# Performance work log

Hardware: AMD Instinct MI355X
Metric: run time of the kernel (lower is better)

The kernel has to match this reference:

```python
import jax, jax.numpy as jnp
import numpy as np

B = 4
N = 300000
GRIDS = [(64, 48, 8), (32, 24, 4), (16, 12, 2), (8, 6, 1)]
W_IMG = 640
EFF_R = 2.0 * (int(0.01 * W_IMG + 2) / W_IMG)  # 0.025, as in source
MAXV = [EFF_R, 2.0 * EFF_R, 2.0 / 24.0, 2.0 / 12.0, 2.0 / 6.0]
CIN = [3, 18, 66, 130, 130]
COUT = [16, 64, 128, 128, 128]
E_CNT = [3600000, 786432, 196608, 24576, 3072]
V_CNT = [N, 98304, 12288, 1536, 192]


def cartesian(pos, src, dst, max_value):
    # PyG Cartesian(norm=True, cat=False, max_value=mv) followed by clamp(0,1)
    cart = pos[dst] - pos[src]
    return jnp.clip(cart / (2.0 * max_value) + 0.5, 0.0, 1.0)


def spline_conv(x, src, dst, pseudo, Wk, Wr, b, num_nodes):
    # SplineConv, kernel_size=2, degree=1 B-spline over 3-D pseudo coords:
    # 8 corner weights, per-edge trilinear basis, mean aggregation + root + bias.
    p, q = pseudo, 1.0 - pseudo
    xs = x[src]  # [E, Cin] gather
    msg = jnp.zeros((src.shape[0], Wk.shape[-1]), x.dtype)
    for s in range(8):
        basis = ((p[:, 0] if s & 1 else q[:, 0])
                 * (p[:, 1] if s & 2 else q[:, 1])
                 * (p[:, 2] if s & 4 else q[:, 2]))
        msg = msg + basis[:, None] * (xs @ Wk[s])
    agg = jax.ops.segment_sum(msg, dst, num_segments=num_nodes)
    deg = jax.ops.segment_sum(jnp.ones((dst.shape[0],), x.dtype), dst, num_segments=num_nodes)
    out = agg / jnp.maximum(deg, 1.0)[:, None] + x @ Wr + b
    return jax.nn.relu(out)


def voxel_pool(x, pos, batch, grid, aggr):
    nx, ny, nt = grid
    ix = jnp.clip(jnp.floor(pos[:, 0] * nx).astype(jnp.int32), 0, nx - 1)
    iy = jnp.clip(jnp.floor(pos[:, 1] * ny).astype(jnp.int32), 0, ny - 1)
    it = jnp.clip(jnp.floor(pos[:, 2] * nt).astype(jnp.int32), 0, nt - 1)
    cluster = ((batch * nx + ix) * ny + iy) * nt + it
    V = B * nx * ny * nt
    ones = jnp.ones((x.shape[0],), x.dtype)
    cnt = jax.ops.segment_sum(ones, cluster, num_segments=V)
    posp = jax.ops.segment_sum(pos, cluster, num_segments=V) / jnp.maximum(cnt, 1.0)[:, None]
    if aggr == 'max':
        xp = jax.ops.segment_max(x, cluster, num_segments=V)
        xp = jnp.where(cnt[:, None] > 0, xp, 0.0)
    else:
        xp = jax.ops.segment_sum(x, cluster, num_segments=V) / jnp.maximum(cnt, 1.0)[:, None]
    batchp = jnp.arange(V, dtype=jnp.int32) // (nx * ny * nt)
    return xp, posp, batchp


def _forward(x, pos, batch, edges, params):
    e0 = edges[0]
    ea = cartesian(pos, e0[0], e0[1], MAXV[0])
    h = jnp.concatenate([x, pos[:, :2]], axis=1)
    Wk, Wr, bb = params[0]
    h = spline_conv(h, e0[0], e0[1], ea, Wk, Wr, bb, x.shape[0])
    h, pos, batch = voxel_pool(h, pos, batch, GRIDS[0], 'max')
    out3 = None
    for i in range(4):
        e = edges[i + 1]
        ea = cartesian(pos, e[0], e[1], MAXV[i + 1])
        h = jnp.concatenate([h, pos[:, :2]], axis=1)
        Wk, Wr, bb = params[i + 1]
        h = spline_conv(h, e[0], e[1], ea, Wk, Wr, bb, pos.shape[0])
        if i == 2:
            out3 = h  # features after layer4 (out3 scale)
        if i < 3:
            h, pos, batch = voxel_pool(h, pos, batch, GRIDS[i + 1], 'max' if i < 2 else 'mean')
    return out3, h


def setup_inputs() -> dict:
    key = jax.random.key(0)
    ks = jax.random.split(key, 40)
    inp = {}
    inp['x'] = jax.random.uniform(ks[0], (N, 1), dtype=jnp.float32)
    inp['pos'] = jax.random.uniform(ks[1], (N, 3), dtype=jnp.float32)
    inp['batch'] = jnp.sort(jax.random.randint(ks[2], (N,), 0, B, dtype=jnp.int32))
    for i in range(5):
        inp[f'e{i}'] = jax.random.randint(ks[3 + i], (2, E_CNT[i]), 0, V_CNT[i], dtype=jnp.int32)
    kidx = 8
    for i in range(5):
        scale = 1.0 / np.sqrt(8.0 * CIN[i])
        inp[f'W{i + 1}'] = scale * jax.random.normal(ks[kidx], (8, CIN[i], COUT[i]), dtype=jnp.float32); kidx += 1
        inp[f'R{i + 1}'] = scale * jax.random.normal(ks[kidx], (CIN[i], COUT[i]), dtype=jnp.float32); kidx += 1
        inp[f'b{i + 1}'] = jnp.zeros((COUT[i],), dtype=jnp.float32)
    return inp


def reference(x, pos, batch, e0, e1, e2, e3, e4,
              W1, R1, b1, W2, R2, b2, W3, R3, b3, W4, R4, b4, W5, R5, b5):
    params = [(W1, R1, b1), (W2, R2, b2), (W3, R3, b3), (W4, R4, b4), (W5, R5, b5)]
    edges = [e0, e1, e2, e3, e4]
    return _forward(x, pos, batch, edges, params)
```

## Files before the change

kernel.cpp:

```cpp
#include <hip/hip_runtime.h>
#include <cstdint>

__device__ __forceinline__ float clamp01f(float v) { return fminf(fmaxf(v, 0.0f), 1.0f); }

__device__ __forceinline__ void basis8(float p0, float p1, float p2, float* bs)
{
    float q0 = 1.f - p0, q1 = 1.f - p1, q2 = 1.f - p2;
    float t00 = q0 * q1, t10 = p0 * q1, t01 = q0 * p1, t11 = p0 * p1;
    bs[0] = t00 * q2; bs[1] = t10 * q2; bs[2] = t01 * q2; bs[3] = t11 * q2;
    bs[4] = t00 * p2; bs[5] = t10 * p2; bs[6] = t01 * p2; bs[7] = t11 * p2;
}

__global__ __launch_bounds__(256) void edge_count_kernel(
    const int* __restrict__ edst, int* __restrict__ cnt, int E)
{
    int e = blockIdx.x * 256 + threadIdx.x;
    if (e < E) atomicAdd(&cnt[__builtin_nontemporal_load(&edst[e])], 1);
}

__global__ __launch_bounds__(256) void edge_scatter_kernel(
    const int* __restrict__ esrc, const int* __restrict__ edst,
    int* __restrict__ off, int* __restrict__ srcs, int E, int rv)
{
    const int lo = (int)(blockIdx.x & 7) * rv;
    const int hi = lo + rv;
    const int base = (int)(blockIdx.x >> 3) << 10;
#pragma unroll
    for (int k = 0; k < 4; ++k) {
        int e = base + (k << 8) + threadIdx.x;
        if (e < E) {
            int d = __builtin_nontemporal_load(&edst[e]);
            if (d >= lo && d < hi) {
                int s = __builtin_nontemporal_load(&esrc[e]);
                int slot = atomicAdd(&off[d], 1);
                srcs[slot] = s;
            }
        }
    }
}

__global__ __launch_bounds__(256) void scan1_kernel(
    const int* __restrict__ cnt, int* __restrict__ off, int* __restrict__ bsum, int V)
{
    __shared__ int lds[4096];
    __shared__ int ssum[256];
    const int t = threadIdx.x;
    const int base = blockIdx.x * 4096;
    for (int i = t; i < 4096; i += 256) {
        int g = base + i;
        lds[i] = (g < V) ? cnt[g] : 0;
    }
    __syncthreads();
    int loc[16];
    int s = 0;
#pragma unroll
    for (int k = 0; k < 16; ++k) { loc[k] = s; s += lds[t * 16 + k]; }
    ssum[t] = s;
    __syncthreads();
    for (int d = 1; d < 256; d <<= 1) {
        int v = (t >= d) ? ssum[t - d] : 0;
        __syncthreads();
        ssum[t] += v;
        __syncthreads();
    }
    const int tbase = (t == 0) ? 0 : ssum[t - 1];
    if (t == 255 && bsum) bsum[blockIdx.x] = ssum[255];
#pragma unroll
    for (int k = 0; k < 16; ++k) lds[t * 16 + k] = tbase + loc[k];
    __syncthreads();
    for (int i = t; i < 4096; i += 256) {
        int g = base + i;
        if (g < V) off[g] = lds[i];
    }
}

__global__ __launch_bounds__(256) void scan_add_kernel(
    int* __restrict__ off, const int* __restrict__ bso, int V)
{
    int g = blockIdx.x * 256 + threadIdx.x;
    if (g < V) off[g] += bso[g >> 12];
}

__global__ __launch_bounds__(256) void bin_count_kernel(
    const int* __restrict__ edst, int* __restrict__ gcnt, int E, int shift)
{
    __shared__ int h[256];
    const int t = threadIdx.x;
    h[t] = 0;
    __syncthreads();
    const int base = blockIdx.x << 12;
#pragma unroll
    for (int k = 0; k < 16; ++k) {
        int e = base + (k << 8) + t;
        if (e < E) {
            int d = __builtin_nontemporal_load(&edst[e]);
            atomicAdd(&h[d >> shift], 1);
        }
    }
    __syncthreads();
    if (h[t]) atomicAdd(&gcnt[t], h[t]);
}

__global__ __launch_bounds__(256) void bin_scatter_kernel(
    const int* __restrict__ esrc, const int* __restrict__ edst,
    int* __restrict__ gcur, int* __restrict__ stD, int* __restrict__ stS,
    int E, int shift)
{
    __shared__ int d_l[4096];
    __shared__ int s_l[4096];
    __shared__ int h[256];
    __shared__ int rbase[256];
    const int t = threadIdx.x;
    h[t] = 0;
    __syncthreads();
    const int base = blockIdx.x << 12;
#pragma unroll
    for (int k = 0; k < 16; ++k) {
        int i = (k << 8) + t;
        int e = base + i;
        if (e < E) {
            int d = __builtin_nontemporal_load(&edst[e]);
            int s = __builtin_nontemporal_load(&esrc[e]);
            d_l[i] = d; s_l[i] = s;
            atomicAdd(&h[d >> shift], 1);
        }
    }
    __syncthreads();
    rbase[t] = h[t] ? atomicAdd(&gcur[t], h[t]) : 0;
    h[t] = 0;
    __syncthreads();
#pragma unroll
    for (int k = 0; k < 16; ++k) {
        int i = (k << 8) + t;
        int e = base + i;
        if (e < E) {
            int d = d_l[i];
            int b = d >> shift;
            int r = atomicAdd(&h[b], 1);
            int pos = rbase[b] + r;
            stD[pos] = d;
            stS[pos] = s_l[i];
        }
    }
}

__global__ __launch_bounds__(1024) void bucket_csr_kernel(
    const int* __restrict__ gcur, const int* __restrict__ gcnt,
    const int* __restrict__ stD, const int* __restrict__ stS,
    int* __restrict__ cnt, int* __restrict__ off, int* __restrict__ srcs,
    int V, int shift)
{
    __shared__ int h[2048];
    __shared__ int o[2048];
    __shared__ int ps[1024];
    const int t = threadIdx.x;
    const int b = blockIdx.x;
    const int v0 = b << shift;
    const int nv = min(1 << shift, V - v0);
    const int s1 = gcur[b];
    const int s0 = s1 - gcnt[b];
    h[t] = 0; h[t + 1024] = 0;
    __syncthreads();
    for (int i = s0 + t; i < s1; i += 1024)
        atomicAdd(&h[stD[i] - v0], 1);
    __syncthreads();
    int a = h[2 * t], b2 = h[2 * t + 1];
    ps[t] = a + b2;
    __syncthreads();
    for (int d = 1; d < 1024; d <<= 1) {
        int v = (t >= d) ? ps[t - d] : 0;
        __syncthreads();
        ps[t] += v;
        __syncthreads();
    }
    int pb = (t == 0) ? 0 : ps[t - 1];
    o[2 * t] = pb;
    o[2 * t + 1] = pb + a;
    __syncthreads();
    for (int i = t; i < nv; i += 1024) {
        int hv = h[i];
        cnt[v0 + i] = hv;
        off[v0 + i] = s0 + o[i] + hv;
    }
    __syncthreads();
    for (int i = s0 + t; i < s1; i += 1024) {
        int d = stD[i];
        int r = atomicAdd(&o[d - v0], 1);
        srcs[s0 + r] = stS[i];
    }
}

__global__ __launch_bounds__(256) void pack_xpos_kernel(
    const float* __restrict__ x, const float* __restrict__ pos,
    float4* __restrict__ xp, int V)
{
    int n = blockIdx.x * 256 + threadIdx.x;
    if (n >= V) return;
    xp[n] = make_float4(x[n], pos[n * 3 + 0], pos[n * 3 + 1], pos[n * 3 + 2]);
}

__device__ __forceinline__ void l1_edge_acc(
    const float4 d, const float4 a, float inv2mv, float ts[8][3])
{
    float p0 = clamp01f((d.y - a.y) * inv2mv + 0.5f);
    float p1 = clamp01f((d.z - a.z) * inv2mv + 0.5f);
    float p2 = clamp01f((d.w - a.w) * inv2mv + 0.5f);
    float bs[8];
    basis8(p0, p1, p2, bs);
#pragma unroll
    for (int s8 = 0; s8 < 8; ++s8) {
        ts[s8][0] += bs[s8] * a.x;
        ts[s8][1] += bs[s8] * a.y;
        ts[s8][2] += bs[s8] * a.z;
    }
}

__global__ __launch_bounds__(256) void l1_fused_kernel(
    const int* __restrict__ off, const int* __restrict__ cnt, const int* __restrict__ srcs,
    const float4* __restrict__ xp,
    const float* __restrict__ Wk, const float* __restrict__ Wr,
    const float* __restrict__ bias, float* __restrict__ out,
    float inv2mv, int V)
{
    __shared__ float sWk[384];
    __shared__ float sWr[48];
    __shared__ float sB[16];
    const int t = threadIdx.x;
    for (int i = t; i < 384; i += 256) sWk[i] = Wk[i];
    if (t < 48) sWr[t] = Wr[t];
    if (t < 16) sB[t] = bias[t];
    __syncthreads();
    const int v = blockIdx.x * 256 + t;
    if (v >= V) return;
    const float4 d = xp[v];
    const int e1 = off[v];
    const int n = cnt[v];
    float ts[8][3];
#pragma unroll
    for (int s8 = 0; s8 < 8; ++s8) { ts[s8][0] = 0.f; ts[s8][1] = 0.f; ts[s8][2] = 0.f; }
    int j = e1 - n;
    for (; j + 3 < e1; j += 4) {
        float4 a0 = xp[srcs[j]];
        float4 a1 = xp[srcs[j + 1]];
        float4 a2 = xp[srcs[j + 2]];
        float4 a3 = xp[srcs[j + 3]];
        l1_edge_acc(d, a0, inv2mv, ts);
        l1_edge_acc(d, a1, inv2mv, ts);
        l1_edge_acc(d, a2, inv2mv, ts);
        l1_edge_acc(d, a3, inv2mv, ts);
    }
    for (; j < e1; ++j)
        l1_edge_acc(d, xp[srcs[j]], inv2mv, ts);
    const float invn = 1.0f / fmaxf((float)n, 1.0f);
    float rr[16];
#pragma unroll
    for (int c = 0; c < 16; ++c) {
        float m = 0.f;
#pragma unroll
        for (int s8 = 0; s8 < 8; ++s8)
            m += ts[s8][0] * sWk[s8 * 48 + c]
               + ts[s8][1] * sWk[s8 * 48 + 16 + c]
               + ts[s8][2] * sWk[s8 * 48 + 32 + c];
        float r = m * invn + d.x * sWr[c] + d.y * sWr[16 + c] + d.z * sWr[32 + c] + sB[c];
        rr[c] = fmaxf(r, 0.0f);
    }
    float4* op = (float4*)(out + (size_t)v * 16);
#pragma unroll
    for (int k = 0; k < 4; ++k)
        op[k] = make_float4(rr[4 * k], rr[4 * k + 1], rr[4 * k + 2], rr[4 * k + 3]);
}

__device__ __forceinline__ void l2_edge_acc(
    const float4 pd, const float4 pa, float fa, int l16, float inv2mv,
    float* accF, float* accP)
{
    float p0 = clamp01f((pd.x - pa.x) * inv2mv + 0.5f);
    float p1 = clamp01f((pd.y - pa.y) * inv2mv + 0.5f);
    float p2 = clamp01f((pd.z - pa.z) * inv2mv + 0.5f);
    float bs[8];
    basis8(p0, p1, p2, bs);
    const float fp = (l16 == 0) ? pa.x : ((l16 == 1) ? pa.y : 0.f);
#pragma unroll
    for (int s8 = 0; s8 < 8; ++s8) {
        accF[s8] += bs[s8] * fa;
        accP[s8] += bs[s8] * fp;
    }
}

template<int NW>
__global__ __launch_bounds__(64 * NW) void tsum16_layer_kernel(
    const int* __restrict__ off, const int* __restrict__ cnt, const int* __restrict__ srcs,
    const float4* __restrict__ pos4, const float* __restrict__ feat,
    const float* __restrict__ Wk, const float* __restrict__ Wr,
    const float* __restrict__ bias, float* __restrict__ out,
    float inv2mv, int V)
{
    __shared__ float tsum[NW][4][18][9];
    const int tid = threadIdx.x;
    const int w = tid >> 6, lane = tid & 63;
    const int q = lane >> 4, l16 = lane & 15;
    const int vbase = (blockIdx.x * NW + w) * 4;
    const int v = vbase + q;

    const float4 pd = pos4[v];
    const int e1 = off[v];
    const int n = cnt[v];
    float accF[8], accP[8];
#pragma unroll
    for (int s8 = 0; s8 < 8; ++s8) { accF[s8] = 0.f; accP[s8] = 0.f; }
    int j = e1 - n;
    for (; j + 3 < e1; j += 4) {
        const int s0 = srcs[j], s1 = srcs[j + 1], s2 = srcs[j + 2], s3 = srcs[j + 3];
        const float4 pa = pos4[s0];
        const float4 pb = pos4[s1];
        const float4 pc = pos4[s2];
        const float4 pe = pos4[s3];
        const float fa = feat[(size_t)s0 * 16 + l16];
        const float fb = feat[(size_t)s1 * 16 + l16];
        const float fc = feat[(size_t)s2 * 16 + l16];
        const float fe = feat[(size_t)s3 * 16 + l16];
        l2_edge_acc(pd, pa, fa, l16, inv2mv, accF, accP);
        l2_edge_acc(pd, pb, fb, l16, inv2mv, accF, accP);
        l2_edge_acc(pd, pc, fc, l16, inv2mv, accF, accP);
        l2_edge_acc(pd, pe, fe, l16, inv2mv, accF, accP);
    }
    for (; j < e1; ++j) {
        const int s = srcs[j];
        const float4 pa = pos4[s];
        const float fa = feat[(size_t)s * 16 + l16];
        l2_edge_acc(pd, pa, fa, l16, inv2mv, accF, accP);
    }
#pragma unroll
    for (int s8 = 0; s8 < 8; ++s8)
        tsum[w][q][l16][s8] = accF[s8];
    tsum[w][q][l16][8] = feat[(size_t)v * 16 + l16];
    if (l16 < 2) {
#pragma unroll
        for (int s8 = 0; s8 < 8; ++s8)
            tsum[w][q][16 + l16][s8] = accP[s8];
        tsum[w][q][16 + l16][8] = (l16 == 0) ? pd.x : pd.y;
    }
    __syncthreads();

    float oA[4], oR[4];
#pragma unroll
    for (int b = 0; b < 4; ++b) { oA[b] = 0.f; oR[b] = 0.f; }
    for (int s8 = 0; s8 < 8; ++s8) {
        const float* W = Wk + (size_t)s8 * 18 * 64;
        for (int ci = 0; ci < 18; ++ci) {
            float wv = W[(size_t)ci * 64 + lane];
#pragma unroll
            for (int b = 0; b < 4; ++b)
                oA[b] += tsum[w][b][ci][s8] * wv;
        }
    }
    for (int ci = 0; ci < 18; ++ci) {
        float wv = Wr[(size_t)ci * 64 + lane];
#pragma unroll
        for (int b = 0; b < 4; ++b)
            oR[b] += tsum[w][b][ci][8] * wv;
    }
    const float bi = bias[lane];
#pragma unroll
    for (int b = 0; b < 4; ++b) {
        int vv = vbase + b;
        float invn = 1.0f / fmaxf((float)cnt[vv], 1.0f);
        out[(size_t)vv * 64 + lane] = fmaxf(oA[b] * invn + oR[b] + bi, 0.0f);
    }
}

template<int CINF, int COUT, int NV, int NW, int PMODE>
__global__ __launch_bounds__(64 * NW) void tsum_layer_kernel(
    const int* __restrict__ off, const int* __restrict__ cnt, const int* __restrict__ srcs,
    const float4* __restrict__ pos4, const float* __restrict__ feat,
    const float* __restrict__ Wk, const float* __restrict__ Wr,
    const float* __restrict__ bias, float* __restrict__ out,
    float* __restrict__ hp, float* __restrict__ psum, float* __restrict__ pcnt,
    float inv2mv, int V, int gx, int gy, int gt, int bdiv)
{
    constexpr int CIN = CINF + 2;
    constexpr int NCI = (CIN + 63) / 64;
    constexpr int NCC = COUT / 64;
    __shared__ float tsum[NW][NV][CIN][9];
    __shared__ int scl[NW][NV];
    const int tid = threadIdx.x;
    const int w = tid >> 6, lane = tid & 63;
    const int vbase = (blockIdx.x * NW + w) * NV;

    for (int b = 0; b < NV; ++b) {
        const int v = vbase + b;
        if (v >= V) break;
        const float4 pd = pos4[v];
        float acc[NCI][8];
#pragma unroll
        for (int k = 0; k < NCI; ++k)
#pragma unroll
            for (int s8 = 0; s8 < 8; ++s8) acc[k][s8] = 0.f;
        const int e1 = off[v];
        int j = e1 - cnt[v];
        for (; j + 1 < e1; j += 2) {
            const int s0 = srcs[j], s1 = srcs[j + 1];
            const float4 pa = pos4[s0];
            const float4 pb = pos4[s1];
            float fa[NCI], fb[NCI];
#pragma unroll
            for (int k = 0; k < NCI; ++k) {
                int ci = lane + 64 * k;
                fa[k] = (ci < CINF) ? feat[(size_t)s0 * CINF + ci]
                       : (ci == CINF ? pa.x : (ci == CINF + 1 ? pa.y : 0.f));
                fb[k] = (ci < CINF) ? feat[(size_t)s1 * CINF + ci]
                       : (ci == CINF ? pb.x : (ci == CINF + 1 ? pb.y : 0.f));
            }
            float pa0 = clamp01f((pd.x - pa.x) * inv2mv + 0.5f);
            float pa1 = clamp01f((pd.y - pa.y) * inv2mv + 0.5f);
            float pa2 = clamp01f((pd.z - pa.z) * inv2mv + 0.5f);
            float pb0 = clamp01f((pd.x - pb.x) * inv2mv + 0.5f);
            float pb1 = clamp01f((pd.y - pb.y) * inv2mv + 0.5f);
            float pb2 = clamp01f((pd.z - pb.z) * inv2mv + 0.5f);
            float ba[8], bb[8];
            basis8(pa0, pa1, pa2, ba);
            basis8(pb0, pb1, pb2, bb);
#pragma unroll
            for (int s8 = 0; s8 < 8; ++s8)
#pragma unroll
                for (int k = 0; k < NCI; ++k)
                    acc[k][s8] += ba[s8] * fa[k] + bb[s8] * fb[k];
        }
        if (j < e1) {
            const int s = srcs[j];
            const float4 pa = pos4[s];
            float fa[NCI];
#pragma unroll
            for (int k = 0; k < NCI; ++k) {
                int ci = lane + 64 * k;
                fa[k] = (ci < CINF) ? feat[(size_t)s * CINF + ci]
                       : (ci == CINF ? pa.x : (ci == CINF + 1 ? pa.y : 0.f));
            }
            float p0 = clamp01f((pd.x - pa.x) * inv2mv + 0.5f);
            float p1 = clamp01f((pd.y - pa.y) * inv2mv + 0.5f);
            float p2 = clamp01f((pd.z - pa.z) * inv2mv + 0.5f);
            float bs[8];
            basis8(p0, p1, p2, bs);
#pragma unroll
            for (int s8 = 0; s8 < 8; ++s8)
#pragma unroll
                for (int k = 0; k < NCI; ++k)
                    acc[k][s8] += bs[s8] * fa[k];
        }
#pragma unroll
        for (int k = 0; k < NCI; ++k) {
            int ci = lane + 64 * k;
            if (ci < CIN) {
#pragma unroll
                for (int s8 = 0; s8 < 8; ++s8)
                    tsum[w][b][ci][s8] = acc[k][s8];
                tsum[w][b][ci][8] = (ci < CINF) ? feat[(size_t)v * CINF + ci]
                                                : (ci == CINF ? pd.x : pd.y);
            }
        }
        if (PMODE != 0 && lane == 0) {
            int bb2 = v / bdiv;
            int ix = min(max((int)floorf(pd.x * (float)gx), 0), gx - 1);
            int iy = min(max((int)floorf(pd.y * (float)gy), 0), gy - 1);
            int it = min(max((int)floorf(pd.z * (float)gt), 0), gt - 1);
            int cl = ((bb2 * gx + ix) * gy + iy) * gt + it;
            scl[w][b] = cl;
            atomicAdd(&psum[cl * 3 + 0], pd.x);
            atomicAdd(&psum[cl * 3 + 1], pd.y);
            atomicAdd(&psum[cl * 3 + 2], pd.z);
            atomicAdd(&pcnt[cl], 1.0f);
        }
    }
    __syncthreads();

    float oA[NV][NCC], oR[NV][NCC];
#pragma unroll
    for (int b = 0; b < NV; ++b)
#pragma unroll
        for (int cc = 0; cc < NCC; ++cc) { oA[b][cc] = 0.f; oR[b][cc] = 0.f; }
    for (int s8 = 0; s8 < 8; ++s8) {
        const float* W = Wk + (size_t)s8 * CIN * COUT;
        for (int ci = 0; ci < CIN; ++ci) {
            float wv[NCC];
#pragma unroll
            for (int cc = 0; cc < NCC; ++cc)
                wv[cc] = W[(size_t)ci * COUT + cc * 64 + lane];
#pragma unroll
            for (int b = 0; b < NV; ++b) {
                float tv = tsum[w][b][ci][s8];
#pragma unroll
                for (int cc = 0; cc < NCC; ++cc) oA[b][cc] += tv * wv[cc];
            }
        }
    }
    for (int ci = 0; ci < CIN; ++ci) {
        float wv[NCC];
#pragma unroll
        for (int cc = 0; cc < NCC; ++cc)
            wv[cc] = Wr[(size_t)ci * COUT + cc * 64 + lane];
#pragma unroll
        for (int b = 0; b < NV; ++b) {
            float tv = tsum[w][b][ci][8];
#pragma unroll
            for (int cc = 0; cc < NCC; ++cc) oR[b][cc] += tv * wv[cc];
        }
    }
    for (int b = 0; b < NV; ++b) {
        int v = vbase + b;
        if (v >= V) break;
        float invn = 1.0f / fmaxf((float)cnt[v], 1.0f);
#pragma unroll
        for (int cc = 0; cc < NCC; ++cc) {
            int c = cc * 64 + lane;
            float val = fmaxf(oA[b][cc] * invn + oR[b][cc] + bias[c], 0.0f);
            if (PMODE == 0 || PMODE == 2)
                out[(size_t)v * COUT + c] = val;
            if (PMODE == 1)
                atomicMax((int*)&hp[(size_t)scl[w][b] * COUT + c], __float_as_int(val));
            if (PMODE == 2)
                atomicAdd(&hp[(size_t)scl[w][b] * COUT + c], val);
        }
    }
}

__global__ __launch_bounds__(256) void pool_cluster_kernel(
    const float* __restrict__ p4, int ofs, const int* __restrict__ batch, int bdiv, int V,
    int nx, int ny, int nt, int* __restrict__ cl, int* __restrict__ cnt)
{
    int n = blockIdx.x * 256 + threadIdx.x;
    if (n >= V) return;
    int b = batch ? batch[n] : (n / bdiv);
    const float* pp = p4 + (size_t)n * 4 + ofs;
    float px = pp[0], py = pp[1], pt = pp[2];
    int ix = (int)floorf(px * (float)nx); ix = min(max(ix, 0), nx - 1);
    int iy = (int)floorf(py * (float)ny); iy = min(max(iy, 0), ny - 1);
    int it = (int)floorf(pt * (float)nt); it = min(max(it, 0), nt - 1);
    int c = ((b * nx + ix) * ny + iy) * nt + it;
    cl[n] = c;
    atomicAdd(&cnt[c], 1);
}

__global__ __launch_bounds__(256) void pool_scatter_kernel(
    const int* __restrict__ cl, int* __restrict__ off, int* __restrict__ order, int V, int rv)
{
    const int lo = (int)(blockIdx.x & 7) * rv;
    const int hi = lo + rv;
    const int base = (int)(blockIdx.x >> 3) << 10;
#pragma unroll
    for (int k = 0; k < 4; ++k) {
        int n = base + (k << 8) + threadIdx.x;
        if (n < V) {
            int c = __builtin_nontemporal_load(&cl[n]);
            if (c >= lo && c < hi) {
                int slot = atomicAdd(&off[c], 1);
                order[slot] = n;
            }
        }
    }
}

template<int COUT>
__global__ __launch_bounds__(256) void staged_pool_kernel(
    const int* __restrict__ order, const int* __restrict__ cl,
    const int* __restrict__ ioff, const int* __restrict__ icnt,
    const float* __restrict__ h, const float* __restrict__ p4, int ofs,
    float* __restrict__ hp, float* __restrict__ psum, int V)
{
    __shared__ float sh[256][COUT + 4];
    __shared__ float sp[256][3];
    __shared__ int scl2[256];
    const int t = threadIdx.x;
    const int w = t >> 6, lane = t & 63;
    const int gbase = blockIdx.x * 256 + w * 64;
    const int slot = gbase + lane;
    int myc = -1;
    if (slot < V) {
        int n = order[slot];
        myc = cl[n];
        const float* hr = h + (size_t)n * COUT;
#pragma unroll
        for (int k = 0; k < COUT / 4; ++k)
            *(float4*)&sh[w * 64 + lane][k * 4] = *(const float4*)&hr[k * 4];
        const float* pp = p4 + (size_t)n * 4 + ofs;
        sp[w * 64 + lane][0] = pp[0];
        sp[w * 64 + lane][1] = pp[1];
        sp[w * 64 + lane][2] = pp[2];
    }
    scl2[w * 64 + lane] = myc;
    __syncthreads();

    if (lane < COUT) {
        const int c = lane;
        const int sb = w * 64;
        int prev = scl2[sb];
        float run = 0.f, rp = 0.f;
        for (int i = 0; i < 64; ++i) {
            int cc = scl2[sb + i];
            if (cc != prev) {
                if (prev >= 0) {
                    int en = ioff[prev];
                    int st = en - icnt[prev];
                    if (st >= gbase && en <= gbase + 64) {
                        hp[(size_t)prev * COUT + c] = run;
                        if (c < 3) psum[prev * 3 + c] = rp;
                    } else {
                        atomicMax((int*)&hp[(size_t)prev * COUT + c], __float_as_int(run));
                        if (c < 3) atomicAdd(&psum[prev * 3 + c], rp);
                    }
                }
                prev = cc; run = 0.f; rp = 0.f;
            }
            if (cc >= 0) {
                run = fmaxf(run, sh[sb + i][c]);
                if (c < 3) rp += sp[sb + i][c];
            }
        }
        if (prev >= 0) {
            int en = ioff[prev];
            int st = en - icnt[prev];
            if (st >= gbase && en <= gbase + 64) {
                hp[(size_t)prev * COUT + c] = run;
                if (c < 3) psum[prev * 3 + c] = rp;
            } else {
                atomicMax((int*)&hp[(size_t)prev * COUT + c], __float_as_int(run));
                if (c < 3) atomicAdd(&psum[prev * 3 + c], rp);
            }
        }
    }
}

__global__ __launch_bounds__(256) void finalize_posI_kernel(
    const float* __restrict__ psum, const int* __restrict__ icnt,
    float4* __restrict__ pos_out, int Vc)
{
    int c = blockIdx.x * 256 + threadIdx.x;
    if (c >= Vc) return;
    float m = fmaxf((float)icnt[c], 1.0f);
    pos_out[c] = make_float4(psum[c * 3 + 0] / m, psum[c * 3 + 1] / m,
                             psum[c * 3 + 2] / m, 0.f);
}

__global__ __launch_bounds__(256) void finalize_pos_kernel(
    const float* __restrict__ psum, const float* __restrict__ pcnt,
    float4* __restrict__ pos_out, int Vc)
{
    int c = blockIdx.x * 256 + threadIdx.x;
    if (c >= Vc) return;
    float m = fmaxf(pcnt[c], 1.0f);
    pos_out[c] = make_float4(psum[c * 3 + 0] / m, psum[c * 3 + 1] / m,
                             psum[c * 3 + 2] / m, 0.f);
}

__global__ __launch_bounds__(256) void finalize_mean_kernel(
    const float* __restrict__ hsum, const float* __restrict__ psum,
    const float* __restrict__ pcnt,
    float* __restrict__ hout, float4* __restrict__ pos_out, int Vc)
{
    int g = blockIdx.x * 256 + threadIdx.x;
    if (g >= Vc * 128) return;
    int c = g >> 7, ch = g & 127;
    float m = fmaxf(pcnt[c], 1.0f);
    hout[g] = hsum[g] / m;
    if (ch == 0)
        pos_out[c] = make_float4(psum[c * 3 + 0] / m, psum[c * 3 + 1] / m,
                                 psum[c * 3 + 2] / m, 0.f);
}

extern "C" void kernel_launch(void* const* d_in, const int* in_sizes, int n_in,
                              void* d_out, int out_size, void* d_ws, size_t ws_size,
                              hipStream_t stream)
{
    (void)in_sizes; (void)n_in; (void)out_size;
    const float* x    = (const float*)d_in[0];
    const float* pos0 = (const float*)d_in[1];
    const int*   bat  = (const int*)d_in[2];
    const int* e1 = (const int*)d_in[3];
    const int* e2 = (const int*)d_in[4];
    const int* e3 = (const int*)d_in[5];
    const int* e4 = (const int*)d_in[6];
    const int* e5 = (const int*)d_in[7];
    const float* W1 = (const float*)d_in[8],  *R1 = (const float*)d_in[9],  *B1 = (const float*)d_in[10];
    const float* W2 = (const float*)d_in[11], *R2 = (const float*)d_in[12], *B2 = (const float*)d_in[13];
    const float* W3 = (const float*)d_in[14], *R3 = (const float*)d_in[15], *B3 = (const float*)d_in[16];
    const float* W4 = (const float*)d_in[17], *R4 = (const float*)d_in[18], *B4 = (const float*)d_in[19];
    const float* W5 = (const float*)d_in[20], *R5 = (const float*)d_in[21], *B5 = (const float*)d_in[22];

    const int E1 = 3600000, E2 = 786432, E3 = 196608, E4 = 24576, E5 = 3072;

    if (ws_size < (size_t)21800000 * sizeof(float)) return;
    float* ws = (float*)d_ws;
    float* P0 = ws;
    float* P1 = ws + 12600000;
    float* P2 = ws + 18900000;
    int*   P3 = (int*)(ws + 20500000);
    float* P4 = ws + 21500000;
    int* GCNT   = P3 + 990000;
    int* GCUR   = P3 + 990256;
    int* SCR_BS = P3 + 999744;
    int* SCR_BO = SCR_BS + 96;

    float* out3 = (float*)d_out;
    float* hfin = (float*)d_out + 196608;

#define MSI(p, ni) hipMemsetAsync((p), 0, (size_t)(ni) * sizeof(int), stream)

#define SCAN(cntp, offp, Vn)                                                                     \
    {                                                                                            \
        int nb_ = ((Vn) + 4095) / 4096;                                                          \
        if (nb_ <= 1) {                                                                          \
            scan1_kernel<<<1, 256, 0, stream>>>((cntp), (offp), nullptr, (Vn));                  \
        } else {                                                                                 \
            scan1_kernel<<<nb_, 256, 0, stream>>>((cntp), (offp), SCR_BS, (Vn));                 \
            scan1_kernel<<<1, 256, 0, stream>>>(SCR_BS, SCR_BO, nullptr, nb_);                   \
            scan_add_kernel<<<((Vn) + 255) / 256, 256, 0, stream>>>((offp), SCR_BO, (Vn));       \
        }                                                                                        \
    }

#define BSORT(cntP, offP, srcP, stD, stS, ep, En, Vn, SHIFT, NB)                                 \
    {                                                                                            \
        MSI(GCNT, 256);                                                                          \
        bin_count_kernel<<<((En) + 4095) / 4096, 256, 0, stream>>>((ep) + (En), GCNT, En, SHIFT);\
        scan1_kernel<<<1, 256, 0, stream>>>(GCNT, GCUR, nullptr, NB);                            \
        bin_scatter_kernel<<<((En) + 4095) / 4096, 256, 0, stream>>>(                            \
            (ep), (ep) + (En), GCUR, stD, stS, En, SHIFT);                                       \
        bucket_csr_kernel<<<NB, 1024, 0, stream>>>(                                              \
            GCUR, GCNT, stD, stS, cntP, offP, srcP, Vn, SHIFT);                                  \
    }

#define ESORT(base, ep, En, Vn)                                                                  \
    int* cnt_ = (base);                                                                          \
    int* off_ = cnt_ + (Vn);                                                                     \
    int* src_ = off_ + (Vn);                                                                     \
    MSI(cnt_, (Vn));                                                                             \
    edge_count_kernel<<<((En) + 255) / 256, 256, 0, stream>>>((ep) + (En), cnt_, En);            \
    SCAN(cnt_, off_, (Vn));                                                                      \
    edge_scatter_kernel<<<8 * (((En) + 1023) / 1024), 256, 0, stream>>>(                         \
        (ep), (ep) + (En), off_, src_, En, (Vn) >> 3)

#define SPOOL(ICLp, IORDp, ICNTp, IOFFp, p4src, ofsv, batp, bdiv, Vn, Vc, NX, NY, NT, COUTV, \
              hsrc, hpool, psumP, posdst)                                                   \
    {                                                                                       \
        MSI(ICNTp, (Vc));                                                                   \
        pool_cluster_kernel<<<((Vn) + 255) / 256, 256, 0, stream>>>(                        \
            p4src, ofsv, batp, bdiv, Vn, NX, NY, NT, ICLp, ICNTp);                          \
        SCAN(ICNTp, IOFFp, (Vc));                                                           \
        pool_scatter_kernel<<<8 * (((Vn) + 1023) / 1024), 256, 0, stream>>>(                \
            ICLp, IOFFp, IORDp, Vn, (Vc) >> 3);                                             \
        MSI(hpool, (size_t)(Vc) * (COUTV));                                                 \
        MSI(psumP, (size_t)(Vc) * 3);                                                       \
        staged_pool_kernel<COUTV><<<((Vn) + 255) / 256, 256, 0, stream>>>(                  \
            IORDp, ICLp, IOFFp, ICNTp, hsrc, p4src, ofsv, hpool, psumP, Vn);                \
        finalize_posI_kernel<<<((Vc) + 255) / 256, 256, 0, stream>>>(                       \
            psumP, ICNTp, (float4*)(posdst), Vc);                                           \
    }

    {
        int* cnt1 = (int*)P0;
        int* off1 = cnt1 + 300000;
        int* src1 = off1 + 300000;
        int* stD  = src1 + 3600000;
        int* stS  = stD + 3600000;
        float4* xp4 = (float4*)(P0 + 11400000);
        BSORT(cnt1, off1, src1, stD, stS, e1, E1, 300000, 11, 147);
        pack_xpos_kernel<<<(300000 + 255) / 256, 256, 0, stream>>>(x, pos0, xp4, 300000);
        l1_fused_kernel<<<(300000 + 255) / 256, 256, 0, stream>>>(
            off1, cnt1, src1, xp4, W1, R1, B1, P1, 20.0f, 300000);
        int* ICL1  = P3;
        int* IORD1 = P3 + 300000;
        int* ICNT1 = P3 + 600000;
        int* IOFF1 = P3 + 698304;
        SPOOL(ICL1, IORD1, ICNT1, IOFF1, (const float*)xp4, 1, bat, 0, 300000, 98304,
              64, 48, 8, 16, P1, P2, P0, P0 + 300000);
    }
    float4* pos2_4 = (float4*)(P0 + 300000);
    {
        int* cnt2 = P3;
        int* off2 = cnt2 + 98304;
        int* src2 = off2 + 98304;
        int* stD  = (int*)(P0 + 1000000);
        int* stS  = stD + E2;
        BSORT(cnt2, off2, src2, stD, stS, e2, E2, 98304, 10, 96);
        tsum16_layer_kernel<4><<<98304 / 16, 256, 0, stream>>>(
            off2, cnt2, src2, pos2_4, P2, W2, R2, B2, P1, 10.0f, 98304);
        int* ICL2  = P3;
        int* IORD2 = P3 + 98304;
        int* ICNT2 = P3 + 196608;
        int* IOFF2 = P3 + 208896;
        SPOOL(ICL2, IORD2, ICNT2, IOFF2, (const float*)pos2_4, 0, nullptr, 24576,
              98304, 12288, 32, 24, 4, 64, P1, P2, P2 + 786432, P4);
    }
    {
        ESORT(P3, e3, E3, 12288);
        float* HP3 = P1;
        float* PS3 = P1 + 196608;
        float* PC3 = P1 + 201216;
        MSI(P1, 202752);
        tsum_layer_kernel<64, 128, 4, 4, 1><<<12288 / 16, 256, 0, stream>>>(
            off_, cnt_, src_, (const float4*)P4, P2, W3, R3, B3, nullptr,
            HP3, PS3, PC3, 6.0f, 12288, 16, 12, 2, 3072);
        finalize_pos_kernel<<<(1536 + 255) / 256, 256, 0, stream>>>(
            PS3, PC3, (float4*)P0, 1536);
    }
    {
        ESORT(P3, e4, E4, 1536);
        float* HS4 = P2;
        float* PS4 = P2 + 24576;
        float* PC4 = P2 + 25152;
        MSI(P2, 25344);
        tsum_layer_kernel<128, 128, 2, 4, 2><<<1536 / 8, 256, 0, stream>>>(
            off_, cnt_, src_, (const float4*)P0, P1, W4, R4, B4, out3,
            HS4, PS4, PC4, 3.0f, 1536, 8, 6, 1, 384);
        finalize_mean_kernel<<<(192 * 128 + 255) / 256, 256, 0, stream>>>(
            HS4, PS4, PC4, P1, (float4*)(P0 + 100000), 192);
    }
    {
        ESORT(P3, e5, E5, 192);
        tsum_layer_kernel<128, 128, 2, 4, 0><<<192 / 8, 256, 0, stream>>>(
            off_, cnt_, src_, (const float4*)(P0 + 100000), P1, W5, R5, B5, hfin,
            nullptr, nullptr, nullptr, 1.5f, 192, 1, 1, 1, 1);
    }
#undef SPOOL
#undef ESORT
#undef BSORT
#undef SCAN
#undef MSI
}
```

Baseline: 858.7 us.

## Interleave staged edge pairs, stage layer-2 weights in LDS, use 32-bit indexing

```diff
diff --git a/kernel.cpp b/kernel.cpp
--- a/kernel.cpp
+++ b/kernel.cpp
@@ -103,8 +103,7 @@
 
 __global__ __launch_bounds__(256) void bin_scatter_kernel(
     const int* __restrict__ esrc, const int* __restrict__ edst,
-    int* __restrict__ gcur, int* __restrict__ stD, int* __restrict__ stS,
-    int E, int shift)
+    int* __restrict__ gcur, int2* __restrict__ st, int E, int shift)
 {
     __shared__ int d_l[4096];
     __shared__ int s_l[4096];
@@ -137,16 +136,14 @@
             int d = d_l[i];
             int b = d >> shift;
             int r = atomicAdd(&h[b], 1);
-            int pos = rbase[b] + r;
-            stD[pos] = d;
-            stS[pos] = s_l[i];
+            st[rbase[b] + r] = make_int2(d, s_l[i]);
         }
     }
 }
 
 __global__ __launch_bounds__(1024) void bucket_csr_kernel(
     const int* __restrict__ gcur, const int* __restrict__ gcnt,
-    const int* __restrict__ stD, const int* __restrict__ stS,
+    const int2* __restrict__ st,
     int* __restrict__ cnt, int* __restrict__ off, int* __restrict__ srcs,
     int V, int shift)
 {
@@ -162,7 +159,7 @@
     h[t] = 0; h[t + 1024] = 0;
     __syncthreads();
     for (int i = s0 + t; i < s1; i += 1024)
-        atomicAdd(&h[stD[i] - v0], 1);
+        atomicAdd(&h[st[i].x - v0], 1);
     __syncthreads();
     int a = h[2 * t], b2 = h[2 * t + 1];
     ps[t] = a + b2;
@@ -184,9 +181,9 @@
     }
     __syncthreads();
     for (int i = s0 + t; i < s1; i += 1024) {
-        int d = stD[i];
-        int r = atomicAdd(&o[d - v0], 1);
-        srcs[s0 + r] = stS[i];
+        int2 e = st[i];
+        int r = atomicAdd(&o[e.x - v0], 1);
+        srcs[s0 + r] = e.y;
     }
 }
 
@@ -295,12 +292,19 @@
     const float* __restrict__ bias, float* __restrict__ out,
     float inv2mv, int V)
 {
+    __shared__ float sW[8 * 18 * 64];
+    __shared__ float sR[18 * 64];
+    __shared__ float sB2[64];
     __shared__ float tsum[NW][4][18][9];
     const int tid = threadIdx.x;
     const int w = tid >> 6, lane = tid & 63;
     const int q = lane >> 4, l16 = lane & 15;
     const int vbase = (blockIdx.x * NW + w) * 4;
     const int v = vbase + q;
+
+    for (int i = tid; i < 9216; i += 64 * NW) sW[i] = Wk[i];
+    for (int i = tid; i < 1152; i += 64 * NW) sR[i] = Wr[i];
+    if (tid < 64) sB2[tid] = bias[tid];
 
     const float4 pd = pos4[v];
     const int e1 = off[v];
@@ -315,10 +319,10 @@
         const float4 pb = pos4[s1];
         const float4 pc = pos4[s2];
         const float4 pe = pos4[s3];
-        const float fa = feat[(size_t)s0 * 16 + l16];
-        const float fb = feat[(size_t)s1 * 16 + l16];
-        const float fc = feat[(size_t)s2 * 16 + l16];
-        const float fe = feat[(size_t)s3 * 16 + l16];
+        const float fa = feat[s0 * 16 + l16];
+        const float fb = feat[s1 * 16 + l16];
+        const float fc = feat[s2 * 16 + l16];
+        const float fe = feat[s3 * 16 + l16];
         l2_edge_acc(pd, pa, fa, l16, inv2mv, accF, accP);
         l2_edge_acc(pd, pb, fb, l16, inv2mv, accF, accP);
         l2_edge_acc(pd, pc, fc, l16, inv2mv, accF, accP);
@@ -327,13 +331,13 @@
     for (; j < e1; ++j) {
         const int s = srcs[j];
         const float4 pa = pos4[s];
-        const float fa = feat[(size_t)s * 16 + l16];
+        const float fa = feat[s * 16 + l16];
         l2_edge_acc(pd, pa, fa, l16, inv2mv, accF, accP);
     }
 #pragma unroll
     for (int s8 = 0; s8 < 8; ++s8)
         tsum[w][q][l16][s8] = accF[s8];
-    tsum[w][q][l16][8] = feat[(size_t)v * 16 + l16];
+    tsum[w][q][l16][8] = feat[v * 16 + l16];
     if (l16 < 2) {
 #pragma unroll
         for (int s8 = 0; s8 < 8; ++s8)
@@ -346,21 +350,21 @@
 #pragma unroll
     for (int b = 0; b < 4; ++b) { oA[b] = 0.f; oR[b] = 0.f; }
     for (int s8 = 0; s8 < 8; ++s8) {
-        const float* W = Wk + (size_t)s8 * 18 * 64;
+        const float* W = sW + s8 * (18 * 64);
         for (int ci = 0; ci < 18; ++ci) {
-            float wv = W[(size_t)ci * 64 + lane];
+            float wv = W[ci * 64 + lane];
 #pragma unroll
             for (int b = 0; b < 4; ++b)
                 oA[b] += tsum[w][b][ci][s8] * wv;
         }
     }
     for (int ci = 0; ci < 18; ++ci) {
-        float wv = Wr[(size_t)ci * 64 + lane];
+        float wv = sR[ci * 64 + lane];
 #pragma unroll
         for (int b = 0; b < 4; ++b)
             oR[b] += tsum[w][b][ci][8] * wv;
     }
-    const float bi = bias[lane];
+    const float bi = sB2[lane];
 #pragma unroll
     for (int b = 0; b < 4; ++b) {
         int vv = vbase + b;
@@ -406,9 +410,9 @@
 #pragma unroll
             for (int k = 0; k < NCI; ++k) {
                 int ci = lane + 64 * k;
-                fa[k] = (ci < CINF) ? feat[(size_t)s0 * CINF + ci]
+                fa[k] = (ci < CINF) ? feat[s0 * CINF + ci]
                        : (ci == CINF ? pa.x : (ci == CINF + 1 ? pa.y : 0.f));
-                fb[k] = (ci < CINF) ? feat[(size_t)s1 * CINF + ci]
+                fb[k] = (ci < CINF) ? feat[s1 * CINF + ci]
                        : (ci == CINF ? pb.x : (ci == CINF + 1 ? pb.y : 0.f));
             }
             float pa0 = clamp01f((pd.x - pa.x) * inv2mv + 0.5f);
@@ -433,7 +437,7 @@
 #pragma unroll
             for (int k = 0; k < NCI; ++k) {
                 int ci = lane + 64 * k;
-                fa[k] = (ci < CINF) ? feat[(size_t)s * CINF + ci]
+                fa[k] = (ci < CINF) ? feat[s * CINF + ci]
                        : (ci == CINF ? pa.x : (ci == CINF + 1 ? pa.y : 0.f));
             }
             float p0 = clamp01f((pd.x - pa.x) * inv2mv + 0.5f);
@@ -454,7 +458,7 @@
 #pragma unroll
                 for (int s8 = 0; s8 < 8; ++s8)
                     tsum[w][b][ci][s8] = acc[k][s8];
-                tsum[w][b][ci][8] = (ci < CINF) ? feat[(size_t)v * CINF + ci]
+                tsum[w][b][ci][8] = (ci < CINF) ? feat[v * CINF + ci]
                                                 : (ci == CINF ? pd.x : pd.y);
             }
         }
@@ -716,15 +720,15 @@
         }                                                                                        \
     }
 
-#define BSORT(cntP, offP, srcP, stD, stS, ep, En, Vn, SHIFT, NB)                                 \
+#define BSORT(cntP, offP, srcP, stP, ep, En, Vn, SHIFT, NB)                                      \
     {                                                                                            \
         MSI(GCNT, 256);                                                                          \
         bin_count_kernel<<<((En) + 4095) / 4096, 256, 0, stream>>>((ep) + (En), GCNT, En, SHIFT);\
         scan1_kernel<<<1, 256, 0, stream>>>(GCNT, GCUR, nullptr, NB);                            \
         bin_scatter_kernel<<<((En) + 4095) / 4096, 256, 0, stream>>>(                            \
-            (ep), (ep) + (En), GCUR, stD, stS, En, SHIFT);                                       \
+            (ep), (ep) + (En), GCUR, stP, En, SHIFT);                                            \
         bucket_csr_kernel<<<NB, 1024, 0, stream>>>(                                              \
-            GCUR, GCNT, stD, stS, cntP, offP, srcP, Vn, SHIFT);                                  \
+            GCUR, GCNT, stP, cntP, offP, srcP, Vn, SHIFT);                                       \
     }
 
 #define ESORT(base, ep, En, Vn)                                                                  \
@@ -758,10 +762,9 @@
         int* cnt1 = (int*)P0;
         int* off1 = cnt1 + 300000;
         int* src1 = off1 + 300000;
-        int* stD  = src1 + 3600000;
-        int* stS  = stD + 3600000;
+        int2* st1 = (int2*)(src1 + 3600000);
         float4* xp4 = (float4*)(P0 + 11400000);
-        BSORT(cnt1, off1, src1, stD, stS, e1, E1, 300000, 11, 147);
+        BSORT(cnt1, off1, src1, st1, e1, E1, 300000, 11, 147);
         pack_xpos_kernel<<<(300000 + 255) / 256, 256, 0, stream>>>(x, pos0, xp4, 300000);
         l1_fused_kernel<<<(300000 + 255) / 256, 256, 0, stream>>>(
             off1, cnt1, src1, xp4, W1, R1, B1, P1, 20.0f, 300000);
@@ -777,9 +780,8 @@
         int* cnt2 = P3;
         int* off2 = cnt2 + 98304;
         int* src2 = off2 + 98304;
-        int* stD  = (int*)(P0 + 1000000);
-        int* stS  = stD + E2;
-        BSORT(cnt2, off2, src2, stD, stS, e2, E2, 98304, 10, 96);
+        int2* st2 = (int2*)(P0 + 1000000);
+        BSORT(cnt2, off2, src2, st2, e2, E2, 98304, 10, 96);
         tsum16_layer_kernel<4><<<98304 / 16, 256, 0, stream>>>(
             off2, cnt2, src2, pos2_4, P2, W2, R2, B2, P1, 10.0f, 98304);
         int* ICL2  = P3;
```

Measured after the change: 870.4 us. About the same (+1.4%).
